# Kernel optimization log

Hardware: AMD Instinct MI355X
Metric: run time of the kernel (lower is better)

Reference implementation:

```python
import jax, jax.numpy as jnp
import numpy as np

H = 4  # heads (init_kwargs)
E = 64  # embed_size
D = E // H
PREC_DIM = 2
FF = 4 * E


def _layernorm(x, g, b, eps=1e-5):
    mu = jnp.mean(x, axis=-1, keepdims=True)
    var = jnp.mean((x - mu) ** 2, axis=-1, keepdims=True)
    return (x - mu) * jax.lax.rsqrt(var + eps) * g + b


def setup_inputs() -> dict:
    key = jax.random.key(0)
    ks = jax.random.split(key, 16)
    B, S, N = 128, 192, 32
    s = 0.05
    return {
        "precedence": jax.random.normal(ks[0], (B, S, N, PREC_DIM), dtype=jnp.float32),
        "top_mask": jax.random.randint(ks[1], (B, N), 0, 2, dtype=jnp.int32),
        "We": jax.random.normal(ks[2], (PREC_DIM, E), dtype=jnp.float32) * s,
        "be": jnp.zeros((E,), jnp.float32),
        "Wq": jax.random.normal(ks[3], (D, D), dtype=jnp.float32) * s,
        "Wk": jax.random.normal(ks[4], (D, D), dtype=jnp.float32) * s,
        "Wv": jax.random.normal(ks[5], (D, D), dtype=jnp.float32) * s,
        "Wo": jax.random.normal(ks[6], (E, E), dtype=jnp.float32) * s,
        "bo": jnp.zeros((E,), jnp.float32),
        "ln1_g": jnp.ones((E,), jnp.float32),
        "ln1_b": jnp.zeros((E,), jnp.float32),
        "W1": jax.random.normal(ks[7], (E, FF), dtype=jnp.float32) * s,
        "b1": jnp.zeros((FF,), jnp.float32),
        "W2": jax.random.normal(ks[8], (FF, E), dtype=jnp.float32) * s,
        "b2": jnp.zeros((E,), jnp.float32),
        "ln2_g": jnp.ones((E,), jnp.float32),
        "ln2_b": jnp.zeros((E,), jnp.float32),
    }


def reference(precedence, top_mask, We, be, Wq, Wk, Wv, Wo, bo,
              ln1_g, ln1_b, W1, b1, W2, b2, ln2_g, ln2_b):
    B, S, N, _ = precedence.shape
    M = B * S
    # embedding: [B,S,N,E]
    pv = precedence @ We + be
    # gather-indexed query: prec_vecs[:, s, s % box_num]
    sidx = jnp.arange(S)
    q = pv[:, sidx, sidx % N]                      # [B,S,E]
    vals = pv.reshape(M, N, E)                     # values == keys
    qr = q.reshape(M, 1, E)
    # mask: [B,1,1,N] expanded over states -> [M,1,1,N]
    mask = jnp.broadcast_to(top_mask[:, None, None, None, :], (B, S, 1, 1, N)).reshape(M, 1, 1, N)
    # per-head linear projections (shared across heads)
    vh = vals.reshape(M, N, H, D) @ Wv
    kh = vals.reshape(M, N, H, D) @ Wk
    qh = qr.reshape(M, 1, H, D) @ Wq
    energy = jnp.einsum("mqhd,mkhd->mhqk", qh, kh)           # [M,H,1,N]
    energy = jnp.where(mask == 0, jnp.float32(-1e20), energy)
    attn = jax.nn.softmax(energy / jnp.sqrt(jnp.float32(E)), axis=-1)
    oh = jnp.einsum("mhqk,mkhd->mqhd", attn, vh).reshape(M, 1, E)
    ao = oh @ Wo + bo
    x = _layernorm(ao + qr, ln1_g, ln1_b)
    ff = jax.nn.relu(x @ W1 + b1) @ W2 + b2
    out = _layernorm(ff + x, ln2_g, ln2_b)
    return out.reshape(B, S, E)
```

## Files before the change

### kernel.cpp

```cpp
#include <hip/hip_runtime.h>
#include <math.h>

namespace {

constexpr int S_  = 192;
constexpr int TPW = 8;
constexpr int WVB = 4;

__device__ __forceinline__ void wave_fence() {
  asm volatile("s_waitcnt lgkmcnt(0)" ::: "memory");
}

__launch_bounds__(256)
__attribute__((amdgpu_waves_per_eu(4, 4)))
__global__ void prec_fused(
    const float* __restrict__ prec,  const int*   __restrict__ tmask,
    const float* __restrict__ We,    const float* __restrict__ be,
    const float* __restrict__ Wq,    const float* __restrict__ Wk,
    const float* __restrict__ Wv,    const float* __restrict__ Wo,
    const float* __restrict__ bo,    const float* __restrict__ g1,
    const float* __restrict__ bb1,   const float* __restrict__ W1,
    const float* __restrict__ b1,    const float* __restrict__ W2,
    const float* __restrict__ b2,    const float* __restrict__ g2,
    const float* __restrict__ bb2,   float* __restrict__ out)
{
  __shared__ __align__(16) float sh[WVB][2048];
  __shared__ __align__(16) float sxoh[WVB][TPW][64];

  const int tid  = threadIdx.x;
  const int wv   = tid >> 6;
  const int lane = tid & 63;
  const int u    = lane >> 5;
  const int n    = lane & 31;
  const int tokbase = (blockIdx.x * WVB + wv) * TPW;
  const int bidx0 = tokbase / S_;
  const int srow0 = tokbase - bidx0 * S_;

  float* __restrict__ sc = &sh[0][0];

  if (tid < 64) { sc[tid] = We[tid]; sc[64 + tid] = We[64 + tid]; sc[128 + tid] = be[tid]; }
  sc[192 + tid] = Wq[tid];
  sc[448 + tid] = Wk[tid];
  sc[704 + tid] = Wv[tid];
  __syncthreads();

  {
    const int sel = tid >> 6;
    if (sel < 3) {
      const int h = (tid >> 4) & 3, c = tid & 15;
      const float* Wm = sc + 192 + sel * 256;
      float a0 = 0.f, a1 = 0.f, a2 = 0.f;
      #pragma unroll
      for (int dp = 0; dp < 16; ++dp) {
        const float w = Wm[dp * 16 + c];
        a0 = fmaf(sc[h * 16 + dp],        w, a0);
        a1 = fmaf(sc[64 + h * 16 + dp],   w, a1);
        a2 = fmaf(sc[128 + h * 16 + dp],  w, a2);
      }
      const int base = 960 + sel * 192 + h * 48 + c;
      sc[base] = a0; sc[base + 16] = a1; sc[base + 32] = a2;
    }
  }
  __syncthreads();

  if (tid < 36) {
    const int h = tid / 9, ab = tid - h * 9, a = ab / 3, b = ab - a * 3;
    const float* Tp = sc + 960  + h * 48 + a * 16;
    const float* Kp = sc + 1152 + h * 48 + b * 16;
    float s = 0.f;
    #pragma unroll
    for (int c = 0; c < 16; ++c) s = fmaf(Tp[c], Kp[c], s);
    sc[1536 + tid] = s;
  }
  {
    const int e = tid & 63, h = tid >> 6;
    const float* Vp = sc + 1344 + h * 48;
    float q0 = 0.f, q1 = 0.f, q2 = 0.f;
    #pragma unroll
    for (int dp = 0; dp < 16; ++dp) {
      const float wo = Wo[(h * 16 + dp) * 64 + e];
      q0 = fmaf(Vp[dp],      wo, q0);
      q1 = fmaf(Vp[16 + dp], wo, q1);
      q2 = fmaf(Vp[32 + dp], wo, q2);
    }
    sc[1600 + (h * 3 + 0) * 64 + e] = q0;
    sc[1600 + (h * 3 + 1) * 64 + e] = q1;
    sc[1600 + (h * 3 + 2) * 64 + e] = q2;
  }
  __syncthreads();

  float m0[9], m1[9];
  #pragma unroll
  for (int i = 0; i < 9; ++i) {
    m0[i] = sc[1536 + (2 * u) * 9 + i];
    m1[i] = sc[1536 + (2 * u + 1) * 9 + i];
  }
  const int hoA = 2 * u, hoB = 2 * u + 1, htA = 2 - 2 * u, htB = 3 - 2 * u;
  float gO0[2], gO1[2], gT0[2], gT1[2];
  #pragma unroll
  for (int a = 0; a < 2; ++a) {
    gO0[a] = sc[1600 + (hoA * 3 + a) * 64 + lane];
    gO1[a] = sc[1600 + (hoB * 3 + a) * 64 + lane];
    gT0[a] = sc[1600 + (htA * 3 + a) * 64 + lane];
    gT1[a] = sc[1600 + (htB * 3 + a) * 64 + lane];
  }
  float c0 = bo[lane];
  #pragma unroll
  for (int h = 0; h < 4; ++h) c0 += sc[1600 + (h * 3 + 2) * 64 + lane];
  const float we0l = sc[lane], we1l = sc[64 + lane], bel = sc[128 + lane];
  const float g1l = g1[lane], b1l_ = bb1[lane];
  const bool masked = (tmask[bidx0 * 32 + n] == 0);
  const bool allm   = (__all((int)masked) != 0);
  __syncthreads();

  #pragma unroll 2
  for (int p = 0; p < TPW; ++p) {
    const int m     = tokbase + p;
    const int nstar = (srow0 + p) & 31;

    const float qx = prec[(size_t)m * 64 + nstar * 2];
    const float qy = prec[(size_t)m * 64 + nstar * 2 + 1];
    const float2 pin = *(const float2*)(prec + (size_t)m * 64 + n * 2);

    const float cA0 = fmaf(qy, m0[3], fmaf(qx, m0[0], m0[6]));
    const float cB0 = fmaf(qy, m0[4], fmaf(qx, m0[1], m0[7]));
    const float cC0 = fmaf(qy, m0[5], fmaf(qx, m0[2], m0[8]));
    const float cA1 = fmaf(qy, m1[3], fmaf(qx, m1[0], m1[6]));
    const float cB1 = fmaf(qy, m1[4], fmaf(qx, m1[1], m1[7]));
    const float cC1 = fmaf(qy, m1[5], fmaf(qx, m1[2], m1[8]));
    const float en0 = fmaf(pin.y, cB0, fmaf(pin.x, cA0, cC0)) * 0.125f;
    const float en1 = fmaf(pin.y, cB1, fmaf(pin.x, cA1, cC1)) * 0.125f;

    float pe0, pe1;
    if (allm) { pe0 = 1.f; pe1 = 1.f; }
    else {
      pe0 = masked ? 0.f : __expf(en0);
      pe1 = masked ? 0.f : __expf(en1);
    }

    float r0 = pe0 * pin.x, r1 = pe0 * pin.y, r2 = pe0;
    float r3 = pe1 * pin.x, r4 = pe1 * pin.y, r5 = pe1;
    #pragma unroll
    for (int o = 1; o < 32; o <<= 1) {
      r0 += __shfl_xor(r0, o, 64); r1 += __shfl_xor(r1, o, 64);
      r2 += __shfl_xor(r2, o, 64); r3 += __shfl_xor(r3, o, 64);
      r4 += __shfl_xor(r4, o, 64); r5 += __shfl_xor(r5, o, 64);
    }
    const float o0 = __shfl_xor(r0, 32, 64), o1 = __shfl_xor(r1, 32, 64);
    const float o2 = __shfl_xor(r2, 32, 64), o3 = __shfl_xor(r3, 32, 64);
    const float o4 = __shfl_xor(r4, 32, 64), o5 = __shfl_xor(r5, 32, 64);
    const float i0 = __builtin_amdgcn_rcpf(r2), i1 = __builtin_amdgcn_rcpf(r5);
    const float i2 = __builtin_amdgcn_rcpf(o2), i3 = __builtin_amdgcn_rcpf(o5);

    float v = c0;
    v = fmaf(fmaf(r1, gO0[1], r0 * gO0[0]), i0, v);
    v = fmaf(fmaf(r4, gO1[1], r3 * gO1[0]), i1, v);
    v = fmaf(fmaf(o1, gT0[1], o0 * gT0[0]), i2, v);
    v = fmaf(fmaf(o4, gT1[1], o3 * gT1[0]), i3, v);
    v += fmaf(qy, we1l, fmaf(qx, we0l, bel));

    float sm = v, s2 = v * v;
    #pragma unroll
    for (int o = 1; o < 64; o <<= 1) {
      sm += __shfl_xor(sm, o, 64);
      s2 += __shfl_xor(s2, o, 64);
    }
    const float mu  = sm * (1.f / 64.f);
    const float var = s2 * (1.f / 64.f) - mu * mu;
    const float rs  = rsqrtf(var + 1e-5f);
    sxoh[wv][p][lane] = (v - mu) * rs * g1l + b1l_;
  }
  __syncthreads();

  float hacc[TPW][4];
  {
    const float4 b1v = *(const float4*)(b1 + 4 * lane);
    #pragma unroll
    for (int t = 0; t < TPW; ++t) {
      hacc[t][0] = b1v.x; hacc[t][1] = b1v.y; hacc[t][2] = b1v.z; hacc[t][3] = b1v.w;
    }
  }
  #pragma unroll 4
  for (int e4 = 0; e4 < 16; ++e4) {
    float4 wr[4];
    #pragma unroll
    for (int kk = 0; kk < 4; ++kk)
      wr[kk] = *(const float4*)(W1 + (e4 * 4 + kk) * 256 + 4 * lane);
    #pragma unroll
    for (int t = 0; t < TPW; ++t) {
      const float4 xv = *(const float4*)&sxoh[wv][t][e4 * 4];
      hacc[t][0] = fmaf(xv.x, wr[0].x, hacc[t][0]);
      hacc[t][1] = fmaf(xv.x, wr[0].y, hacc[t][1]);
      hacc[t][2] = fmaf(xv.x, wr[0].z, hacc[t][2]);
      hacc[t][3] = fmaf(xv.x, wr[0].w, hacc[t][3]);
      hacc[t][0] = fmaf(xv.y, wr[1].x, hacc[t][0]);
      hacc[t][1] = fmaf(xv.y, wr[1].y, hacc[t][1]);
      hacc[t][2] = fmaf(xv.y, wr[1].z, hacc[t][2]);
      hacc[t][3] = fmaf(xv.y, wr[1].w, hacc[t][3]);
      hacc[t][0] = fmaf(xv.z, wr[2].x, hacc[t][0]);
      hacc[t][1] = fmaf(xv.z, wr[2].y, hacc[t][1]);
      hacc[t][2] = fmaf(xv.z, wr[2].z, hacc[t][2]);
      hacc[t][3] = fmaf(xv.z, wr[2].w, hacc[t][3]);
      hacc[t][0] = fmaf(xv.w, wr[3].x, hacc[t][0]);
      hacc[t][1] = fmaf(xv.w, wr[3].y, hacc[t][1]);
      hacc[t][2] = fmaf(xv.w, wr[3].z, hacc[t][2]);
      hacc[t][3] = fmaf(xv.w, wr[3].w, hacc[t][3]);
    }
  }
  float* __restrict__ h1buf = sh[wv];
  #pragma unroll
  for (int t = 0; t < TPW; ++t) {
    float4 hv;
    hv.x = fmaxf(hacc[t][0], 0.f); hv.y = fmaxf(hacc[t][1], 0.f);
    hv.z = fmaxf(hacc[t][2], 0.f); hv.w = fmaxf(hacc[t][3], 0.f);
    *(float4*)&h1buf[t * 256 + 4 * lane] = hv;
  }
  __syncthreads();

  float f2[TPW];
  {
    const float b2l = b2[lane];
    #pragma unroll
    for (int t = 0; t < TPW; ++t) f2[t] = b2l;
  }
  #pragma unroll 4
  for (int f4 = 0; f4 < 64; ++f4) {
    const float w0 = W2[(f4 * 4 + 0) * 64 + lane];
    const float w1 = W2[(f4 * 4 + 1) * 64 + lane];
    const float w2 = W2[(f4 * 4 + 2) * 64 + lane];
    const float w3 = W2[(f4 * 4 + 3) * 64 + lane];
    #pragma unroll
    for (int t = 0; t < TPW; ++t) {
      const float4 hv = *(const float4*)&h1buf[t * 256 + f4 * 4];
      f2[t] = fmaf(hv.x, w0, f2[t]);
      f2[t] = fmaf(hv.y, w1, f2[t]);
      f2[t] = fmaf(hv.z, w2, f2[t]);
      f2[t] = fmaf(hv.w, w3, f2[t]);
    }
  }

  {
    const float g2l = g2[lane], bb2l = bb2[lane];
    #pragma unroll 2
    for (int t = 0; t < TPW; ++t) {
      const float v = f2[t] + sxoh[wv][t][lane];
      float sm = v, s2 = v * v;
      #pragma unroll
      for (int o = 1; o < 64; o <<= 1) {
        sm += __shfl_xor(sm, o, 64);
        s2 += __shfl_xor(s2, o, 64);
      }
      const float mu  = sm * (1.f / 64.f);
      const float var = s2 * (1.f / 64.f) - mu * mu;
      const float rs  = rsqrtf(var + 1e-5f);
      out[(size_t)(tokbase + t) * 64 + lane] = (v - mu) * rs * g2l + bb2l;
    }
  }
}

}

extern "C" void kernel_launch(void* const* d_in, const int* in_sizes, int n_in,
                              void* d_out, int out_size, void* d_ws, size_t ws_size,
                              hipStream_t stream) {
  (void)in_sizes; (void)n_in; (void)d_ws; (void)ws_size; (void)out_size;
  const float* prec = (const float*)d_in[0];
  const int*   tm   = (const int*)  d_in[1];
  const float* We   = (const float*)d_in[2];
  const float* be   = (const float*)d_in[3];
  const float* Wq   = (const float*)d_in[4];
  const float* Wk   = (const float*)d_in[5];
  const float* Wv   = (const float*)d_in[6];
  const float* Wo   = (const float*)d_in[7];
  const float* bo   = (const float*)d_in[8];
  const float* g1   = (const float*)d_in[9];
  const float* bb1  = (const float*)d_in[10];
  const float* W1   = (const float*)d_in[11];
  const float* b1   = (const float*)d_in[12];
  const float* W2   = (const float*)d_in[13];
  const float* b2   = (const float*)d_in[14];
  const float* g2   = (const float*)d_in[15];
  const float* bb2  = (const float*)d_in[16];

  dim3 grid(768), block(256);
  hipLaunchKernelGGL(prec_fused, grid, block, 0, stream,
                     prec, tm, We, be, Wq, Wk, Wv, Wo, bo, g1, bb1,
                     W1, b1, W2, b2, g2, bb2, (float*)d_out);
}
```

Baseline: 140.0 us.

## Split each token group across a wave pair with partial FFN reductions

Each group of 8 tokens is now handled by two waves instead of one. Each wave runs the attention and first LayerNorm for 4 tokens, computes half of the W1 output columns, and does half of the W2 reduction; the two waves swap partial sums through shared memory before the final LayerNorm. The grid is doubled and the waves-per-EU hint is raised from 4 to 6–8. Each wave needs fewer accumulator registers, which should allow more resident waves to hide latency. The cost is repeating the per-block weight-precompute setup twice as often, plus extra barriers and shared-memory traffic for the partial-sum exchange.

```diff
diff --git a/kernel.cpp b/kernel.cpp
--- a/kernel.cpp
+++ b/kernel.cpp
@@ -4,15 +4,15 @@
 namespace {
 
 constexpr int S_  = 192;
-constexpr int TPW = 8;
-constexpr int WVB = 4;
+constexpr int TPP = 8;
+constexpr int PPB = 2;
 
 __device__ __forceinline__ void wave_fence() {
   asm volatile("s_waitcnt lgkmcnt(0)" ::: "memory");
 }
 
 __launch_bounds__(256)
-__attribute__((amdgpu_waves_per_eu(4, 4)))
+__attribute__((amdgpu_waves_per_eu(6, 8)))
 __global__ void prec_fused(
     const float* __restrict__ prec,  const int*   __restrict__ tmask,
     const float* __restrict__ We,    const float* __restrict__ be,
@@ -24,17 +24,19 @@
     const float* __restrict__ b2,    const float* __restrict__ g2,
     const float* __restrict__ bb2,   float* __restrict__ out)
 {
-  __shared__ __align__(16) float sh[WVB][2048];
-  __shared__ __align__(16) float sxoh[WVB][TPW][64];
-
-  const int tid  = threadIdx.x;
-  const int wv   = tid >> 6;
-  const int lane = tid & 63;
-  const int u    = lane >> 5;
-  const int n    = lane & 31;
-  const int tokbase = (blockIdx.x * WVB + wv) * TPW;
-  const int bidx0 = tokbase / S_;
-  const int srow0 = tokbase - bidx0 * S_;
+  __shared__ __align__(16) float sh[PPB][2048];
+  __shared__ __align__(16) float sxoh[PPB][TPP][64];
+
+  const int tid   = threadIdx.x;
+  const int wv    = tid >> 6;
+  const int pairL = wv >> 1;
+  const int w2    = wv & 1;
+  const int lane  = tid & 63;
+  const int u     = lane >> 5;
+  const int n     = lane & 31;
+  const int pairbase = (blockIdx.x * PPB + pairL) * TPP;
+  const int bidx0 = pairbase / S_;
+  const int srow0 = pairbase - bidx0 * S_;
 
   float* __restrict__ sc = &sh[0][0];
 
@@ -45,7 +47,7 @@
   __syncthreads();
 
   {
-    const int sel = tid >> 6;
+    const int sel = wv;
     if (sel < 3) {
       const int h = (tid >> 4) & 3, c = tid & 15;
       const float* Wm = sc + 192 + sel * 256;
@@ -53,9 +55,9 @@
       #pragma unroll
       for (int dp = 0; dp < 16; ++dp) {
         const float w = Wm[dp * 16 + c];
-        a0 = fmaf(sc[h * 16 + dp],        w, a0);
-        a1 = fmaf(sc[64 + h * 16 + dp],   w, a1);
-        a2 = fmaf(sc[128 + h * 16 + dp],  w, a2);
+        a0 = fmaf(sc[h * 16 + dp],       w, a0);
+        a1 = fmaf(sc[64 + h * 16 + dp],  w, a1);
+        a2 = fmaf(sc[128 + h * 16 + dp], w, a2);
       }
       const int base = 960 + sel * 192 + h * 48 + c;
       sc[base] = a0; sc[base + 16] = a1; sc[base + 32] = a2;
@@ -73,7 +75,7 @@
     sc[1536 + tid] = s;
   }
   {
-    const int e = tid & 63, h = tid >> 6;
+    const int e = tid & 63, h = wv;
     const float* Vp = sc + 1344 + h * 48;
     float q0 = 0.f, q1 = 0.f, q2 = 0.f;
     #pragma unroll
@@ -114,9 +116,10 @@
   __syncthreads();
 
   #pragma unroll 2
-  for (int p = 0; p < TPW; ++p) {
-    const int m     = tokbase + p;
-    const int nstar = (srow0 + p) & 31;
+  for (int p = 0; p < 4; ++p) {
+    const int tl    = w2 * 4 + p;
+    const int m     = pairbase + tl;
+    const int nstar = (srow0 + tl) & 31;
 
     const float qx = prec[(size_t)m * 64 + nstar * 2];
     const float qy = prec[(size_t)m * 64 + nstar * 2 + 1];
@@ -168,82 +171,82 @@
     const float mu  = sm * (1.f / 64.f);
     const float var = s2 * (1.f / 64.f) - mu * mu;
     const float rs  = rsqrtf(var + 1e-5f);
-    sxoh[wv][p][lane] = (v - mu) * rs * g1l + b1l_;
-  }
-  __syncthreads();
-
-  float hacc[TPW][4];
-  {
-    const float4 b1v = *(const float4*)(b1 + 4 * lane);
-    #pragma unroll
-    for (int t = 0; t < TPW; ++t) {
-      hacc[t][0] = b1v.x; hacc[t][1] = b1v.y; hacc[t][2] = b1v.z; hacc[t][3] = b1v.w;
-    }
+    sxoh[pairL][tl][lane] = (v - mu) * rs * g1l + b1l_;
+  }
+  __syncthreads();
+
+  const int c2 = 128 * w2 + 2 * lane;
+  float hacc[TPP][2];
+  {
+    const float2 b1v = *(const float2*)(b1 + c2);
+    #pragma unroll
+    for (int t = 0; t < TPP; ++t) { hacc[t][0] = b1v.x; hacc[t][1] = b1v.y; }
   }
   #pragma unroll 4
   for (int e4 = 0; e4 < 16; ++e4) {
-    float4 wr[4];
+    float2 wr[4];
     #pragma unroll
     for (int kk = 0; kk < 4; ++kk)
-      wr[kk] = *(const float4*)(W1 + (e4 * 4 + kk) * 256 + 4 * lane);
-    #pragma unroll
-    for (int t = 0; t < TPW; ++t) {
-      const float4 xv = *(const float4*)&sxoh[wv][t][e4 * 4];
+      wr[kk] = *(const float2*)(W1 + (e4 * 4 + kk) * 256 + c2);
+    #pragma unroll
+    for (int t = 0; t < TPP; ++t) {
+      const float4 xv = *(const float4*)&sxoh[pairL][t][e4 * 4];
       hacc[t][0] = fmaf(xv.x, wr[0].x, hacc[t][0]);
       hacc[t][1] = fmaf(xv.x, wr[0].y, hacc[t][1]);
-      hacc[t][2] = fmaf(xv.x, wr[0].z, hacc[t][2]);
-      hacc[t][3] = fmaf(xv.x, wr[0].w, hacc[t][3]);
       hacc[t][0] = fmaf(xv.y, wr[1].x, hacc[t][0]);
       hacc[t][1] = fmaf(xv.y, wr[1].y, hacc[t][1]);
-      hacc[t][2] = fmaf(xv.y, wr[1].z, hacc[t][2]);
-      hacc[t][3] = fmaf(xv.y, wr[1].w, hacc[t][3]);
       hacc[t][0] = fmaf(xv.z, wr[2].x, hacc[t][0]);
       hacc[t][1] = fmaf(xv.z, wr[2].y, hacc[t][1]);
-      hacc[t][2] = fmaf(xv.z, wr[2].z, hacc[t][2]);
-      hacc[t][3] = fmaf(xv.z, wr[2].w, hacc[t][3]);
       hacc[t][0] = fmaf(xv.w, wr[3].x, hacc[t][0]);
       hacc[t][1] = fmaf(xv.w, wr[3].y, hacc[t][1]);
-      hacc[t][2] = fmaf(xv.w, wr[3].z, hacc[t][2]);
-      hacc[t][3] = fmaf(xv.w, wr[3].w, hacc[t][3]);
-    }
-  }
-  float* __restrict__ h1buf = sh[wv];
-  #pragma unroll
-  for (int t = 0; t < TPW; ++t) {
-    float4 hv;
-    hv.x = fmaxf(hacc[t][0], 0.f); hv.y = fmaxf(hacc[t][1], 0.f);
-    hv.z = fmaxf(hacc[t][2], 0.f); hv.w = fmaxf(hacc[t][3], 0.f);
-    *(float4*)&h1buf[t * 256 + 4 * lane] = hv;
-  }
-  __syncthreads();
-
-  float f2[TPW];
-  {
-    const float b2l = b2[lane];
-    #pragma unroll
-    for (int t = 0; t < TPW; ++t) f2[t] = b2l;
-  }
+    }
+  }
+  float* __restrict__ h1buf = sh[pairL];
+  #pragma unroll
+  for (int t = 0; t < TPP; ++t) {
+    float2 hv;
+    hv.x = fmaxf(hacc[t][0], 0.f);
+    hv.y = fmaxf(hacc[t][1], 0.f);
+    *(float2*)&h1buf[t * 256 + c2] = hv;
+  }
+  wave_fence();
+
+  float f2[TPP];
+  #pragma unroll
+  for (int t = 0; t < TPP; ++t) f2[t] = 0.f;
   #pragma unroll 4
-  for (int f4 = 0; f4 < 64; ++f4) {
+  for (int k = 0; k < 32; ++k) {
+    const int f4 = 32 * w2 + k;
     const float w0 = W2[(f4 * 4 + 0) * 64 + lane];
     const float w1 = W2[(f4 * 4 + 1) * 64 + lane];
-    const float w2 = W2[(f4 * 4 + 2) * 64 + lane];
+    const float w2_ = W2[(f4 * 4 + 2) * 64 + lane];
     const float w3 = W2[(f4 * 4 + 3) * 64 + lane];
     #pragma unroll
-    for (int t = 0; t < TPW; ++t) {
+    for (int t = 0; t < TPP; ++t) {
       const float4 hv = *(const float4*)&h1buf[t * 256 + f4 * 4];
       f2[t] = fmaf(hv.x, w0, f2[t]);
       f2[t] = fmaf(hv.y, w1, f2[t]);
-      f2[t] = fmaf(hv.z, w2, f2[t]);
+      f2[t] = fmaf(hv.z, w2_, f2[t]);
       f2[t] = fmaf(hv.w, w3, f2[t]);
     }
   }
-
-  {
-    const float g2l = g2[lane], bb2l = bb2[lane];
+  __syncthreads();
+
+  float* __restrict__ fpart = h1buf;
+  {
+    const int tb = (1 - w2) * 4;
+    #pragma unroll
+    for (int i = 0; i < 4; ++i)
+      fpart[(tb + i) * 64 + lane] = f2[tb + i];
+  }
+  __syncthreads();
+
+  {
+    const float b2l = b2[lane], g2l = g2[lane], bb2l = bb2[lane];
     #pragma unroll 2
-    for (int t = 0; t < TPW; ++t) {
-      const float v = f2[t] + sxoh[wv][t][lane];
+    for (int i = 0; i < 4; ++i) {
+      const int tl = w2 * 4 + i;
+      const float v = f2[tl] + fpart[tl * 64 + lane] + b2l + sxoh[pairL][tl][lane];
       float sm = v, s2 = v * v;
       #pragma unroll
       for (int o = 1; o < 64; o <<= 1) {
@@ -253,7 +256,7 @@
       const float mu  = sm * (1.f / 64.f);
       const float var = s2 * (1.f / 64.f) - mu * mu;
       const float rs  = rsqrtf(var + 1e-5f);
-      out[(size_t)(tokbase + t) * 64 + lane] = (v - mu) * rs * g2l + bb2l;
+      out[(size_t)(pairbase + tl) * 64 + lane] = (v - mu) * rs * g2l + bb2l;
     }
   }
 }
@@ -282,7 +285,7 @@
   const float* g2   = (const float*)d_in[15];
   const float* bb2  = (const float*)d_in[16];
 
-  dim3 grid(768), block(256);
+  dim3 grid(1536), block(256);
   hipLaunchKernelGGL(prec_fused, grid, block, 0, stream,
                      prec, tm, We, be, Wq, Wk, Wv, Wo, bo, g1, bb1,
                      W1, b1, W2, b2, g2, bb2, (float*)d_out);
```

New measurement: 133.7 us. 1.05x faster.
